# Optimization experiments

Hardware: AMD Instinct MI355X
Metric: run time of the kernel (lower is better)

The kernel has to match this reference:

```python
import jax, jax.numpy as jnp
import numpy as np

D = 512      # model_size
NH = 8       # num_heads
HD = D // NH # head_dim = 64
T = 2048     # seq len (qlen == klen == pos len)
B = 2        # batch

# flattened Bayesian parameter layout (matches flatten_list order in the module)
_SHAPES = [(3 * D, D), (D, D), (D, D), (3 * D,), (D,), (D,), (NH, HD), (NH, HD)]
_N = sum(int(np.prod(s)) for s in _SHAPES)  # 1,314,304


def _unflatten(w):
    out, i = [], 0
    for s in _SHAPES:
        n = int(np.prod(s))
        out.append(w[i:i + n].reshape(s))
        i += n
    return out


def _rel_shift(x):
    # Transformer-XL relative shift: x is [qlen, klen, B, NH]
    q, k, b, n = x.shape
    x = jnp.pad(x, ((0, 0), (1, 0), (0, 0), (0, 0)))  # zero col at front of klen axis
    x = x.reshape(k + 1, q, b, n)[1:]
    return x.reshape(q, k, b, n)


def setup_inputs() -> dict:
    key = jax.random.key(0)
    k1, k2, k3, k4, k5 = jax.random.split(key, 5)
    inp = jax.random.normal(k1, (T, B, D), dtype=jnp.float32)
    pos = jax.random.normal(k2, (T, 1, D), dtype=jnp.float32)
    std = np.sqrt(2.0 / (D + D))
    mu = jax.random.normal(k3, (_N,), dtype=jnp.float32) * std
    rho = -5.0 + 0.1 * jax.random.normal(k4, (_N,), dtype=jnp.float32)
    eps = jax.random.normal(k5, (_N,), dtype=jnp.float32)
    attn_mask = jnp.triu(jnp.ones((T, T), dtype=bool), 1)  # True = masked (future)
    return {"input": inp, "pos": pos, "attn_mask": attn_mask,
            "mu": mu, "rho": rho, "eps": eps}


def reference(input, pos, attn_mask, mu, rho, eps):
    # Gaussian reparameterized weight sample: w = mu + softplus(rho) * eps
    w = mu + jax.nn.softplus(rho) * eps
    (in_w, out_w, pos_w, in_b, out_b, pos_b, r_w_bias, r_r_bias) = _unflatten(w)

    # input projection -> q, k, v : [T, B, NH, HD]
    qkv = input @ in_w.T + in_b                      # [T, B, 3D]
    q, k, v = jnp.split(qkv, 3, axis=-1)
    q = q.reshape(T, B, NH, HD)
    k = k.reshape(T, B, NH, HD)
    v = v.reshape(T, B, NH, HD)

    # relative position projection: [R, NH, HD]
    r = (pos[:, 0, :] @ pos_w.T + pos_b).reshape(-1, NH, HD)

    # content score (AC) and position score (BD) with rel-shift
    AC = jnp.einsum('ibnd,jbnd->ijbn', q + r_w_bias, k)
    BD = _rel_shift(jnp.einsum('ibnd,jnd->ijbn', q + r_r_bias, r))

    scale = np.float32(1.0 / np.sqrt(HD))
    score = (AC + BD) * scale                        # [T, T, B, NH]
    score = jnp.where(attn_mask[:, :, None, None],
                      jnp.finfo(score.dtype).min, score)
    probs = jax.nn.softmax(score, axis=1)

    attn_vec = jnp.einsum('ijbn,jbnd->ibnd', probs, v).reshape(T, B, D)
    return attn_vec @ out_w.T + out_b                # [T, B, D]
```

## Files before the change

### kernel.cpp

```cpp
#include <hip/hip_runtime.h>


typedef float f32x4 __attribute__((ext_vector_type(4)));
typedef short bf16x8 __attribute__((ext_vector_type(8)));

#define NW 1314304
#define OFF_INB  1310720
#define OFF_INW  0
#define OFF_OUTW 786432
#define OFF_POSW 1048576
#define BB_IN  0
#define BB_OUT 1536
#define BB_POS 2048
#define BB_RW  2560
#define BB_RR  3072

#define L2E 1.44269504088896340736f

__device__ __forceinline__ unsigned short f2bf(float x) {
  unsigned u = __builtin_bit_cast(unsigned, x);
  u += 0x7fffu + ((u >> 16) & 1u);
  return (unsigned short)(u >> 16);
}
__device__ __forceinline__ float bf2f(unsigned short s) {
  return __builtin_bit_cast(float, ((unsigned)s) << 16);
}
__device__ __forceinline__ unsigned pk2(float lo, float hi) {
  return (unsigned)f2bf(lo) | ((unsigned)f2bf(hi) << 16);
}

__global__ void prep_kernel(const float* __restrict__ mu, const float* __restrict__ rho,
                            const float* __restrict__ eps,
                            const float* __restrict__ input, const float* __restrict__ pos,
                            unsigned short* __restrict__ Wh, float* __restrict__ Bf,
                            unsigned short* __restrict__ inH, unsigned short* __restrict__ posH) {
  const int bx = blockIdx.x;
  if (bx < 1284) {
    int i = (bx * 256 + threadIdx.x) * 4;
    if (i < NW) {
      float4 m = *(const float4*)&mu[i];
      float4 r = *(const float4*)&rho[i];
      float4 e = *(const float4*)&eps[i];
      float w0 = m.x + ((r.x > 20.f) ? r.x : log1pf(expf(r.x))) * e.x;
      float w1 = m.y + ((r.y > 20.f) ? r.y : log1pf(expf(r.y))) * e.y;
      float w2 = m.z + ((r.z > 20.f) ? r.z : log1pf(expf(r.z))) * e.z;
      float w3 = m.w + ((r.w > 20.f) ? r.w : log1pf(expf(r.w))) * e.w;
      union { unsigned short s[4]; uint2 u; } p;
      p.s[0] = f2bf(w0); p.s[1] = f2bf(w1); p.s[2] = f2bf(w2); p.s[3] = f2bf(w3);
      *(uint2*)&Wh[i] = p.u;
      if (i >= OFF_INB) {
        float4 b; b.x = w0; b.y = w1; b.z = w2; b.w = w3;
        *(float4*)&Bf[i - OFF_INB] = b;
      }
    }
  } else if (bx < 3332) {
    int i = ((bx - 1284) * 256 + threadIdx.x) * 4;
    float4 v = *(const float4*)&input[i];
    union { unsigned short s[4]; uint2 u; } p;
    p.s[0] = f2bf(v.x); p.s[1] = f2bf(v.y); p.s[2] = f2bf(v.z); p.s[3] = f2bf(v.w);
    *(uint2*)&inH[i] = p.u;
  } else {
    int i = ((bx - 3332) * 256 + threadIdx.x) * 4;
    float4 v = *(const float4*)&pos[i];
    union { unsigned short s[4]; uint2 u; } p;
    p.s[0] = f2bf(v.x); p.s[1] = f2bf(v.y); p.s[2] = f2bf(v.z); p.s[3] = f2bf(v.w);
    *(uint2*)&posH[i] = p.u;
  }
}

__device__ __forceinline__ void gemm_loop(const unsigned short* __restrict__ A,
                                          const unsigned short* __restrict__ B,
                                          unsigned short* As, unsigned short* Bs,
                                          f32x4 (&acc)[4]) {
  const int tid = threadIdx.x;
  const int wv = tid >> 6, lane = tid & 63, g = lane >> 4, cc = lane & 15;
  const int row = tid >> 2, q4 = tid & 3;
  const unsigned short* Ap = A + (size_t)row * 512 + 16 * q4;
  const unsigned short* Bp = B + (size_t)row * 512 + 16 * q4;

  *(uint4*)&As[row * 72 + 16 * q4]     = *(const uint4*)Ap;
  *(uint4*)&As[row * 72 + 16 * q4 + 8] = *(const uint4*)(Ap + 8);
  *(uint4*)&Bs[row * 72 + 16 * q4]     = *(const uint4*)Bp;
  *(uint4*)&Bs[row * 72 + 16 * q4 + 8] = *(const uint4*)(Bp + 8);
  __syncthreads();

  for (int it = 0; it < 8; it++) {
    uint4 a0, a1, b0, b1;
    const bool pf = (it < 7);
    if (pf) {
      const unsigned short* An = Ap + 64 * (it + 1);
      const unsigned short* Bn = Bp + 64 * (it + 1);
      a0 = *(const uint4*)An; a1 = *(const uint4*)(An + 8);
      b0 = *(const uint4*)Bn; b1 = *(const uint4*)(Bn + 8);
    }
    __builtin_amdgcn_s_setprio(1);
#pragma unroll
    for (int ks = 0; ks < 2; ks++) {
      bf16x8 af = *(const bf16x8*)&As[(16 * wv + cc) * 72 + 32 * ks + 8 * g];
#pragma unroll
      for (int fn = 0; fn < 4; fn++) {
        bf16x8 bf = *(const bf16x8*)&Bs[(16 * fn + cc) * 72 + 32 * ks + 8 * g];
        acc[fn] = __builtin_amdgcn_mfma_f32_16x16x32_bf16(af, bf, acc[fn], 0, 0, 0);
      }
    }
    __builtin_amdgcn_s_setprio(0);
    __syncthreads();
    if (pf) {
      *(uint4*)&As[row * 72 + 16 * q4]     = a0;
      *(uint4*)&As[row * 72 + 16 * q4 + 8] = a1;
      *(uint4*)&Bs[row * 72 + 16 * q4]     = b0;
      *(uint4*)&Bs[row * 72 + 16 * q4 + 8] = b1;
    }
    __syncthreads();
  }
}

__global__ __launch_bounds__(256, 2)
void gemm01_kernel(const unsigned short* __restrict__ inH, const unsigned short* __restrict__ posH,
                   const unsigned short* __restrict__ Wh, const float* __restrict__ Bf,
                   unsigned short* __restrict__ qrw, unsigned short* __restrict__ qrr,
                   unsigned short* __restrict__ kbuf, unsigned short* __restrict__ vT,
                   unsigned short* __restrict__ rbuf) {
  __shared__ __align__(16) unsigned short As[64 * 72];
  __shared__ __align__(16) unsigned short Bs[64 * 72];
  const int bx = blockIdx.x;
  const int tid = threadIdx.x;
  const int wv = tid >> 6, lane = tid & 63, g = lane >> 4, cc = lane & 15;

  const bool isR = (bx >= 1536);
  int m0, n0;
  const unsigned short *A, *W;
  if (!isR) {
    m0 = (bx & 63) << 6; n0 = (bx >> 6) << 6;
    A = inH + (size_t)m0 * 512;  W = Wh + OFF_INW + (size_t)n0 * 512;
  } else {
    const int t = bx - 1536;
    m0 = (t & 31) << 6; n0 = (t >> 5) << 6;
    A = posH + (size_t)m0 * 512; W = Wh + OFF_POSW + (size_t)n0 * 512;
  }

  f32x4 acc[4];
#pragma unroll
  for (int i = 0; i < 4; i++) { acc[i][0] = 0.f; acc[i][1] = 0.f; acc[i][2] = 0.f; acc[i][3] = 0.f; }
  gemm_loop(A, W, As, Bs, acc);

  const int sec = n0 >> 9;
  if (!isR && sec == 2) {
#pragma unroll
    for (int fn = 0; fn < 4; fn++) {
      const int col = n0 + 16 * fn + cc;
#pragma unroll
      for (int r = 0; r < 4; r++)
        As[(16 * wv + 4 * g + r) * 72 + 16 * fn + cc] = f2bf(acc[fn][r] + Bf[BB_IN + col]);
    }
    __syncthreads();
    const int nh2 = (n0 >> 6) & 7;
#pragma unroll
    for (int cpass = 0; cpass < 2; cpass++) {
      const int ch = tid + cpass * 256;
      const int ncol = ch >> 3, bb2 = (ch >> 2) & 1, jc = ch & 3;
      union { unsigned short s[8]; uint4 u; } pk;
#pragma unroll
      for (int jj = 0; jj < 8; jj++)
        pk.s[jj] = As[(2 * (8 * jc + jj) + bb2) * 72 + ncol];
      *(uint4*)&vT[((size_t)(bb2 * 8 + nh2) * 64 + ncol) * 2048 + (m0 >> 1) + 8 * jc] = pk.u;
    }
    return;
  }

#pragma unroll
  for (int fn = 0; fn < 4; fn++) {
    const int col = n0 + 16 * fn + cc;
#pragma unroll
    for (int r = 0; r < 4; r++) {
      const int mrow = m0 + 16 * wv + 4 * g + r;
      float v = acc[fn][r];
      if (!isR) {
        v += Bf[BB_IN + col];
        const int d = col & 511;
        const int nh = d >> 6, hd = d & 63;
        const int t = mrow >> 1, bb = mrow & 1;
        const size_t bi = ((size_t)(bb * 8 + nh) * 2048 + t) * 64 + hd;
        if (sec == 0) {
          qrw[bi] = f2bf(v + Bf[BB_RW + d]);
          qrr[bi] = f2bf(v + Bf[BB_RR + d]);
        } else {
          kbuf[bi] = f2bf(v);
        }
      } else {
        v += Bf[BB_POS + col];
        rbuf[((size_t)(col >> 6) * 2048 + mrow) * 64 + (col & 63)] = f2bf(v);
      }
    }
  }
}

__global__ __launch_bounds__(256, 2)
void gemmO_kernel(const unsigned short* __restrict__ av, const unsigned short* __restrict__ W,
                  const float* __restrict__ Bf, float* __restrict__ outp) {
  __shared__ __align__(16) unsigned short As[64 * 72];
  __shared__ __align__(16) unsigned short Bs[64 * 72];
  const int bx = blockIdx.x;
  const int tid = threadIdx.x;
  const int wv = tid >> 6, lane = tid & 63, g = lane >> 4, cc = lane & 15;
  const int m0 = (bx & 63) << 6, n0 = (bx >> 6) << 6;

  f32x4 acc[4];
#pragma unroll
  for (int i = 0; i < 4; i++) { acc[i][0] = 0.f; acc[i][1] = 0.f; acc[i][2] = 0.f; acc[i][3] = 0.f; }
  gemm_loop(av + (size_t)m0 * 512, W + (size_t)n0 * 512, As, Bs, acc);

#pragma unroll
  for (int fn = 0; fn < 4; fn++) {
    const int col = n0 + 16 * fn + cc;
#pragma unroll
    for (int r = 0; r < 4; r++) {
      const int mrow = m0 + 16 * wv + 4 * g + r;
      outp[(size_t)mrow * 512 + col] = acc[fn][r] + Bf[BB_OUT + col];
    }
  }
}

__global__ __launch_bounds__(256, 3)
void attn_kernel(const unsigned short* __restrict__ qrw, const unsigned short* __restrict__ qrr,
                 const unsigned short* __restrict__ kb, const unsigned short* __restrict__ vt,
                 const unsigned short* __restrict__ rb, unsigned short* __restrict__ av,
                 unsigned short* __restrict__ pO, float* __restrict__ pStats)
{
  __shared__ __align__(16) unsigned short Ks[64 * 72];
  __shared__ __align__(16) unsigned short Vs[64 * 72];
  __shared__ __align__(16) unsigned short Rs[128 * 72];
  __shared__ __align__(16) unsigned short Gs[4 * 80 * 20];

  const int tid = threadIdx.x;
  const int wv = tid >> 6, lane = tid & 63, g = lane >> 4, cc = lane & 15;
  const int bx = (int)blockIdx.x;
  const int bn = bx & 15;
  const int sid = 79 - (bx >> 4);
  int qt, s, ns;
  if (sid < 8)       { qt = sid;                s = 0;           ns = 1; }
  else if (sid < 24) { qt = 8 + ((sid - 8) >> 1); s = (sid - 8) & 1; ns = 2; }
  else if (sid < 48) { const int t = sid - 24; const int q3 = t / 3; qt = 16 + q3; s = t - 3 * q3; ns = 3; }
  else               { const int t = sid - 48; qt = 24 + (t >> 2); s = t & 3; ns = 4; }
  const int kt0 = s * 8;
  const int kt1 = (kt0 + 8 < qt + 1) ? (kt0 + 8) : (qt + 1);

  const int nh = bn & 7, bb = bn >> 3;
  const int i0 = qt * 64;
  const int i0g = i0 + wv * 16;
  const int w0base = 1984 - i0;

  const size_t qko = (size_t)bn * 2048 * 64;
  const size_t ro = (size_t)nh * 2048 * 64;

  bf16x8 qw[2], qr[2];
#pragma unroll
  for (int ks = 0; ks < 2; ks++) {
    qw[ks] = *(const bf16x8*)&qrw[qko + (size_t)(i0g + cc) * 64 + 32 * ks + 8 * g];
    qr[ks] = *(const bf16x8*)&qrr[qko + (size_t)(i0g + cc) * 64 + 32 * ks + 8 * g];
  }

  float m_run = -3.0e38f, l_run = 0.f;
  f32x4 o[4];
#pragma unroll
  for (int i = 0; i < 4; i++) { o[i][0] = 0.f; o[i][1] = 0.f; o[i][2] = 0.f; o[i][3] = 0.f; }

  const int srow = tid >> 2, sq = tid & 3;
  const int rrow = tid >> 1, rhalf = tid & 1;
  unsigned short* Gw = &Gs[wv * 1600];
  const int rbase = 48 - 16 * wv;

  {
    const unsigned short* kp = &kb[qko + (size_t)(kt0 * 64 + srow) * 64 + 16 * sq];
    *(uint4*)&Ks[srow * 72 + 16 * sq]     = *(const uint4*)kp;
    *(uint4*)&Ks[srow * 72 + 16 * sq + 8] = *(const uint4*)(kp + 8);
    const unsigned short* vp = &vt[qko + (size_t)srow * 2048 + kt0 * 64 + 16 * sq];
    *(uint4*)&Vs[srow * 72 + 16 * sq]     = *(const uint4*)vp;
    *(uint4*)&Vs[srow * 72 + 16 * sq + 8] = *(const uint4*)(vp + 8);
    const int u0 = w0base + kt0 * 64 + rrow;
    const int uc0 = u0 > 2047 ? 2047 : u0;
    const unsigned short* rp = &rb[ro + (size_t)uc0 * 64 + 32 * rhalf];
    unsigned short* rd = &Rs[(u0 & 127) * 72 + 32 * rhalf];
    *(uint4*)rd        = *(const uint4*)rp;
    *(uint4*)(rd + 8)  = *(const uint4*)(rp + 8);
    *(uint4*)(rd + 16) = *(const uint4*)(rp + 16);
    *(uint4*)(rd + 24) = *(const uint4*)(rp + 24);
  }
  __syncthreads();

  for (int kt = kt0; kt < kt1; kt++) {
    const int j0 = kt * 64;
    const int w0k = w0base + j0;
    const bool pf = (kt + 1 < kt1);

    uint4 ka0, ka1, va0, va1, ra0, ra1;
    int rslot = 0;
    if (pf) {
      const unsigned short* kp = &kb[qko + (size_t)(j0 + 64 + srow) * 64 + 16 * sq];
      ka0 = *(const uint4*)kp; ka1 = *(const uint4*)(kp + 8);
      const unsigned short* vp = &vt[qko + (size_t)srow * 2048 + j0 + 64 + 16 * sq];
      va0 = *(const uint4*)vp; va1 = *(const uint4*)(vp + 8);
      const int unew = w0k + 128 + (tid >> 2);
      rslot = unew & 127;
      const int uc = unew > 2047 ? 2047 : unew;
      const unsigned short* rp = &rb[ro + (size_t)uc * 64 + 16 * sq];
      ra0 = *(const uint4*)rp; ra1 = *(const uint4*)(rp + 8);
    }

    f32x4 st[4];
#pragma unroll
    for (int i = 0; i < 4; i++) { st[i][0] = 0.f; st[i][1] = 0.f; st[i][2] = 0.f; st[i][3] = 0.f; }
    __builtin_amdgcn_s_setprio(1);
#pragma unroll
    for (int ks = 0; ks < 2; ks++) {
#pragma unroll
      for (int fm = 0; fm < 4; fm++) {
        bf16x8 ka = *(const bf16x8*)&Ks[(16 * fm + cc) * 72 + 32 * ks + 8 * g];
        st[fm] = __builtin_amdgcn_mfma_f32_16x16x32_bf16(ka, qw[ks], st[fm], 0, 0, 0);
      }
    }
    f32x4 gt[5];
#pragma unroll
    for (int i = 0; i < 5; i++) { gt[i][0] = 0.f; gt[i][1] = 0.f; gt[i][2] = 0.f; gt[i][3] = 0.f; }
    const int rr0 = w0k + rbase + cc;
#pragma unroll
    for (int ks = 0; ks < 2; ks++) {
#pragma unroll
      for (int fm = 0; fm < 5; fm++) {
        const int rrw = (rr0 + 16 * fm) & 127;
        bf16x8 ra = *(const bf16x8*)&Rs[rrw * 72 + 32 * ks + 8 * g];
        gt[fm] = __builtin_amdgcn_mfma_f32_16x16x32_bf16(ra, qr[ks], gt[fm], 0, 0, 0);
      }
    }
    __builtin_amdgcn_s_setprio(0);
#pragma unroll
    for (int fm = 0; fm < 5; fm++)
#pragma unroll
      for (int r = 0; r < 4; r++)
        Gw[(16 * fm + 4 * g + r) * 20 + cc] = f2bf(gt[fm][r]);

    float p[4][4];
    float tm = -3.0e38f;
    const bool diag = (kt == qt);
#pragma unroll
    for (int fm = 0; fm < 4; fm++) {
#pragma unroll
      for (int r = 0; r < 4; r++) {
        const int jj = 16 * fm + 4 * g + r;
        float bd = bf2f(Gw[(jj - cc + 15) * 20 + cc]);
        float sv = (st[fm][r] + bd) * 0.125f;
        if (diag && (jj > cc + 16 * wv)) sv = -3.0e38f;
        p[fm][r] = sv;
        tm = fmaxf(tm, sv);
      }
    }
    tm = fmaxf(tm, __shfl_xor(tm, 16));
    tm = fmaxf(tm, __shfl_xor(tm, 32));
    const float m_new = fmaxf(m_run, tm);
    const float sc = exp2f((m_run - m_new) * L2E);
    float ps = 0.f;
#pragma unroll
    for (int fm = 0; fm < 4; fm++)
#pragma unroll
      for (int r = 0; r < 4; r++) {
        float pv = exp2f((p[fm][r] - m_new) * L2E);
        p[fm][r] = pv;
        ps += pv;
      }
    ps += __shfl_xor(ps, 16);
    ps += __shfl_xor(ps, 32);
    l_run = l_run * sc + ps;
    m_run = m_new;

    float scr[4];
#pragma unroll
    for (int r = 0; r < 4; r++) scr[r] = __shfl(sc, 4 * g + r);
#pragma unroll
    for (int fn = 0; fn < 4; fn++)
#pragma unroll
      for (int r = 0; r < 4; r++) o[fn][r] *= scr[r];

    unsigned u01[4], u23[4];
#pragma unroll
    for (int fm = 0; fm < 4; fm++) {
      u01[fm] = pk2(p[fm][0], p[fm][1]);
      u23[fm] = pk2(p[fm][2], p[fm][3]);
    }
    bf16x8 pa[2];
#pragma unroll
    for (int ks = 0; ks < 2; ks++) {
      union { unsigned u[4]; bf16x8 v; } pw;
#pragma unroll
      for (int j = 0; j < 4; j++) {
        const int srcl = (2 * (g & 1) + (j >> 1)) * 16 + cc;
        unsigned v0 = __shfl((j & 1) ? u23[2 * ks] : u01[2 * ks], srcl);
        unsigned v1 = __shfl((j & 1) ? u23[2 * ks + 1] : u01[2 * ks + 1], srcl);
        pw.u[j] = (g >> 1) ? v1 : v0;
      }
      pa[ks] = pw.v;
    }
    __builtin_amdgcn_s_setprio(1);
#pragma unroll
    for (int ks = 0; ks < 2; ks++) {
#pragma unroll
      for (int fn = 0; fn < 4; fn++) {
        bf16x8 vb = *(const bf16x8*)&Vs[(16 * fn + cc) * 72 + 32 * ks + 8 * g];
        o[fn] = __builtin_amdgcn_mfma_f32_16x16x32_bf16(pa[ks], vb, o[fn], 0, 0, 0);
      }
    }
    __builtin_amdgcn_s_setprio(0);

    __syncthreads();
    if (pf) {
      *(uint4*)&Ks[srow * 72 + 16 * sq]     = ka0;
      *(uint4*)&Ks[srow * 72 + 16 * sq + 8] = ka1;
      *(uint4*)&Vs[srow * 72 + 16 * sq]     = va0;
      *(uint4*)&Vs[srow * 72 + 16 * sq + 8] = va1;
      unsigned short* rd = &Rs[rslot * 72 + 16 * sq];
      *(uint4*)rd       = ra0;
      *(uint4*)(rd + 8) = ra1;
    }
    __syncthreads();
  }

  if (ns == 1) {
    const float inv = 1.0f / l_run;
    float invr[4];
#pragma unroll
    for (int r = 0; r < 4; r++) invr[r] = __shfl(inv, 4 * g + r);
#pragma unroll
    for (int fn = 0; fn < 4; fn++) {
      const int hd = 16 * fn + cc;
#pragma unroll
      for (int r = 0; r < 4; r++) {
        const int irow = i0g + 4 * g + r;
        av[((size_t)(irow * 2 + bb) * 8 + nh) * 64 + hd] = f2bf(o[fn][r] * invr[r]);
      }
    }
  } else {
    const size_t slot = (size_t)(bn * 80 + sid);
#pragma unroll
    for (int fn = 0; fn < 4; fn++) {
      const int hd = 16 * fn + cc;
#pragma unroll
      for (int r = 0; r < 4; r++)
        pO[slot * 4096 + (16 * wv + 4 * g + r) * 64 + hd] = f2bf(o[fn][r]);
    }
    if (g == 0) {
      pStats[slot * 128 + (16 * wv + cc) * 2]     = m_run;
      pStats[slot * 128 + (16 * wv + cc) * 2 + 1] = l_run;
    }
  }
}

__global__ __launch_bounds__(256)
void combine_kernel(const unsigned short* __restrict__ pO, const float* __restrict__ pStats,
                    unsigned short* __restrict__ av) {
  const int bxx = (int)blockIdx.x;
  const int bn = bxx & 15, qt = 8 + (bxx >> 4);
  const int nh = bn & 7, bb = bn >> 3;
  const int ns = (qt >> 3) + 1;
  const int sid0 = (qt < 16) ? (8 + (qt - 8) * 2)
                 : (qt < 24) ? (24 + (qt - 16) * 3)
                             : (48 + (qt - 24) * 4);
  const int tid = threadIdx.x;
  const int ql = tid >> 2, hq = tid & 3;
  const size_t sb = (size_t)(bn * 80 + sid0);

  float M = -3.0e38f;
  for (int i = 0; i < ns; i++)
    M = fmaxf(M, pStats[(sb + i) * 128 + ql * 2]);

  float L = 0.f;
  float accv[16];
#pragma unroll
  for (int j = 0; j < 16; j++) accv[j] = 0.f;
  for (int i = 0; i < ns; i++) {
    const float mi = pStats[(sb + i) * 128 + ql * 2];
    const float li = pStats[(sb + i) * 128 + ql * 2 + 1];
    const float w = exp2f((mi - M) * L2E);
    L += w * li;
    union { uint4 u; unsigned short s[8]; } c0, c1;
    const unsigned short* src = &pO[(sb + i) * 4096 + ql * 64 + 16 * hq];
    c0.u = *(const uint4*)src;
    c1.u = *(const uint4*)(src + 8);
#pragma unroll
    for (int j = 0; j < 8; j++) accv[j]     += w * bf2f(c0.s[j]);
#pragma unroll
    for (int j = 0; j < 8; j++) accv[8 + j] += w * bf2f(c1.s[j]);
  }
  const float inv = 1.0f / L;
  union { uint4 u; unsigned short s[8]; } o0, o1;
#pragma unroll
  for (int j = 0; j < 8; j++) o0.s[j] = f2bf(accv[j] * inv);
#pragma unroll
  for (int j = 0; j < 8; j++) o1.s[j] = f2bf(accv[8 + j] * inv);
  const int q = qt * 64 + ql;
  unsigned short* dst = &av[((size_t)(q * 2 + bb) * 8 + nh) * 64 + 16 * hq];
  *(uint4*)dst       = o0.u;
  *(uint4*)(dst + 8) = o1.u;
}

extern "C" void kernel_launch(void* const* d_in, const int* in_sizes, int n_in,
                              void* d_out, int out_size, void* d_ws, size_t ws_size,
                              hipStream_t stream) {
  const float* input = (const float*)d_in[0];
  const float* pos   = (const float*)d_in[1];
  const float* mu  = (const float*)d_in[3];
  const float* rho = (const float*)d_in[4];
  const float* eps = (const float*)d_in[5];
  float* out = (float*)d_out;

  char* ws = (char*)d_ws;
  unsigned short* Wh   = (unsigned short*)ws;
  float*          Bf   = (float*)(ws + 2628608);
  unsigned short* inH  = (unsigned short*)(ws + 2642944);
  unsigned short* posH = (unsigned short*)(ws + 6837248);
  unsigned short* qrw  = (unsigned short*)(ws + 8934400);
  unsigned short* qrr  = (unsigned short*)(ws + 13128704);
  unsigned short* kbuf = (unsigned short*)(ws + 17323008);
  unsigned short* vT   = (unsigned short*)(ws + 21517312);
  unsigned short* rbuf = (unsigned short*)(ws + 25711616);
  unsigned short* pO   = (unsigned short*)(ws + 27808768);
  float*          pSt  = (float*)(ws + 38294528);
  unsigned short* av   = inH;

  prep_kernel<<<dim3(4356), dim3(256), 0, stream>>>(mu, rho, eps, input, pos, Wh, Bf, inH, posH);
  gemm01_kernel<<<dim3(1792), dim3(256), 0, stream>>>(inH, posH, Wh, Bf, qrw, qrr, kbuf, vT, rbuf);
  attn_kernel<<<dim3(1280), dim3(256), 0, stream>>>(qrw, qrr, kbuf, vT, rbuf, av, pO, pSt);
  combine_kernel<<<dim3(384), dim3(256), 0, stream>>>(pO, pSt, av);
  gemmO_kernel<<<dim3(512), dim3(256), 0, stream>>>(av, Wh + OFF_OUTW, Bf, out);
}
```

Measured before the change: 174.6 us.

## Stage QKV/R epilogue through LDS and swap shuffles for LDS relayout in attention

The projection GEMM epilogue now writes q (with both position biases), k and r tiles into shared memory first and then stores them with coalesced 16-byte writes, in place of scattered 2-byte stores. The 1/sqrt(d) scale is folded into the q tensors there, so the attention inner loop no longer multiplies scores. In the attention kernel the BD tile is stored transposed with packed 8-byte writes and read back with 32-bit loads plus a shift for the relative offset. The P-matrix relayout for the PV MFMA now goes through per-wave LDS instead of many cross-lane shuffles. The cost is extra LDS traffic, a barrier in the epilogue, and a slightly different rounding point because the scale is applied before the bf16 conversion.

```diff
diff --git a/kernel.cpp b/kernel.cpp
--- a/kernel.cpp
+++ b/kernel.cpp
@@ -144,17 +144,63 @@
   for (int i = 0; i < 4; i++) { acc[i][0] = 0.f; acc[i][1] = 0.f; acc[i][2] = 0.f; acc[i][3] = 0.f; }
   gemm_loop(A, W, As, Bs, acc);
 
-  const int sec = n0 >> 9;
-  if (!isR && sec == 2) {
+  const int nh2 = (n0 >> 6) & 7;
+  const int sec = isR ? 3 : (n0 >> 9);
+
+  if (sec == 0) {
 #pragma unroll
     for (int fn = 0; fn < 4; fn++) {
       const int col = n0 + 16 * fn + cc;
+      const float b0 = Bf[BB_IN + col];
+      const float brw = Bf[BB_RW + col], brr = Bf[BB_RR + col];
+#pragma unroll
+      for (int r = 0; r < 4; r++) {
+        const int ml = 16 * wv + 4 * g + r;
+        As[ml * 72 + 16 * fn + cc] = f2bf((acc[fn][r] + b0 + brw) * 0.125f);
+        Bs[ml * 72 + 16 * fn + cc] = f2bf((acc[fn][r] + b0 + brr) * 0.125f);
+      }
+    }
+    __syncthreads();
+    const int t0 = m0 >> 1;
+#pragma unroll
+    for (int pass = 0; pass < 2; pass++) {
+      const int ch = tid + pass * 256;
+      const int bb2 = ch >> 8, tl = (ch >> 3) & 31, hc = ch & 7;
+      const int ml = 2 * tl + bb2;
+      uint4 v1 = *(const uint4*)&As[ml * 72 + 8 * hc];
+      uint4 v2 = *(const uint4*)&Bs[ml * 72 + 8 * hc];
+      const size_t dst = ((size_t)(bb2 * 8 + nh2) * 2048 + t0 + tl) * 64 + 8 * hc;
+      *(uint4*)&qrw[dst] = v1;
+      *(uint4*)&qrr[dst] = v2;
+    }
+  } else if (sec == 1) {
+#pragma unroll
+    for (int fn = 0; fn < 4; fn++) {
+      const int col = n0 + 16 * fn + cc;
+      const float b0 = Bf[BB_IN + col];
+#pragma unroll
+      for (int r = 0; r < 4; r++)
+        As[(16 * wv + 4 * g + r) * 72 + 16 * fn + cc] = f2bf(acc[fn][r] + b0);
+    }
+    __syncthreads();
+    const int t0 = m0 >> 1;
+#pragma unroll
+    for (int pass = 0; pass < 2; pass++) {
+      const int ch = tid + pass * 256;
+      const int bb2 = ch >> 8, tl = (ch >> 3) & 31, hc = ch & 7;
+      const int ml = 2 * tl + bb2;
+      uint4 v1 = *(const uint4*)&As[ml * 72 + 8 * hc];
+      *(uint4*)&kbuf[((size_t)(bb2 * 8 + nh2) * 2048 + t0 + tl) * 64 + 8 * hc] = v1;
+    }
+  } else if (sec == 2) {
+#pragma unroll
+    for (int fn = 0; fn < 4; fn++) {
+      const int col = n0 + 16 * fn + cc;
 #pragma unroll
       for (int r = 0; r < 4; r++)
         As[(16 * wv + 4 * g + r) * 72 + 16 * fn + cc] = f2bf(acc[fn][r] + Bf[BB_IN + col]);
     }
     __syncthreads();
-    const int nh2 = (n0 >> 6) & 7;
 #pragma unroll
     for (int cpass = 0; cpass < 2; cpass++) {
       const int ch = tid + cpass * 256;
@@ -165,32 +211,22 @@
         pk.s[jj] = As[(2 * (8 * jc + jj) + bb2) * 72 + ncol];
       *(uint4*)&vT[((size_t)(bb2 * 8 + nh2) * 64 + ncol) * 2048 + (m0 >> 1) + 8 * jc] = pk.u;
     }
-    return;
-  }
-
-#pragma unroll
-  for (int fn = 0; fn < 4; fn++) {
-    const int col = n0 + 16 * fn + cc;
-#pragma unroll
-    for (int r = 0; r < 4; r++) {
-      const int mrow = m0 + 16 * wv + 4 * g + r;
-      float v = acc[fn][r];
-      if (!isR) {
-        v += Bf[BB_IN + col];
-        const int d = col & 511;
-        const int nh = d >> 6, hd = d & 63;
-        const int t = mrow >> 1, bb = mrow & 1;
-        const size_t bi = ((size_t)(bb * 8 + nh) * 2048 + t) * 64 + hd;
-        if (sec == 0) {
-          qrw[bi] = f2bf(v + Bf[BB_RW + d]);
-          qrr[bi] = f2bf(v + Bf[BB_RR + d]);
-        } else {
-          kbuf[bi] = f2bf(v);
-        }
-      } else {
-        v += Bf[BB_POS + col];
-        rbuf[((size_t)(col >> 6) * 2048 + mrow) * 64 + (col & 63)] = f2bf(v);
-      }
+  } else {
+#pragma unroll
+    for (int fn = 0; fn < 4; fn++) {
+      const int col = n0 + 16 * fn + cc;
+      const float b0 = Bf[BB_POS + col];
+#pragma unroll
+      for (int r = 0; r < 4; r++)
+        As[(16 * wv + 4 * g + r) * 72 + 16 * fn + cc] = f2bf(acc[fn][r] + b0);
+    }
+    __syncthreads();
+#pragma unroll
+    for (int pass = 0; pass < 2; pass++) {
+      const int ch = tid + pass * 256;
+      const int ml = ch >> 3, hc = ch & 7;
+      uint4 v1 = *(const uint4*)&As[ml * 72 + 8 * hc];
+      *(uint4*)&rbuf[((size_t)nh2 * 2048 + m0 + ml) * 64 + 8 * hc] = v1;
     }
   }
 }
@@ -230,7 +266,7 @@
   __shared__ __align__(16) unsigned short Ks[64 * 72];
   __shared__ __align__(16) unsigned short Vs[64 * 72];
   __shared__ __align__(16) unsigned short Rs[128 * 72];
-  __shared__ __align__(16) unsigned short Gs[4 * 80 * 20];
+  __shared__ __align__(16) unsigned short GPs[4 * 16 * 84];
 
   const int tid = threadIdx.x;
   const int wv = tid >> 6, lane = tid & 63, g = lane >> 4, cc = lane & 15;
@@ -267,7 +303,7 @@
 
   const int srow = tid >> 2, sq = tid & 3;
   const int rrow = tid >> 1, rhalf = tid & 1;
-  unsigned short* Gw = &Gs[wv * 1600];
+  unsigned short* Gw = &GPs[wv * 1344];
   const int rbase = 48 - 16 * wv;
 
   {
@@ -333,26 +369,48 @@
       }
     }
     __builtin_amdgcn_s_setprio(0);
-#pragma unroll
-    for (int fm = 0; fm < 5; fm++)
-#pragma unroll
-      for (int r = 0; r < 4; r++)
-        Gw[(16 * fm + 4 * g + r) * 20 + cc] = f2bf(gt[fm][r]);
+
+#pragma unroll
+    for (int fm = 0; fm < 5; fm++) {
+      uint2 w;
+      w.x = pk2(gt[fm][0], gt[fm][1]);
+      w.y = pk2(gt[fm][2], gt[fm][3]);
+      *(uint2*)&Gw[cc * 84 + 16 * fm + 4 * g] = w;
+    }
 
     float p[4][4];
     float tm = -3.0e38f;
     const bool diag = (kt == qt);
+    const int c00 = 15 - cc + 4 * g;
 #pragma unroll
     for (int fm = 0; fm < 4; fm++) {
-#pragma unroll
-      for (int r = 0; r < 4; r++) {
-        const int jj = 16 * fm + 4 * g + r;
-        float bd = bf2f(Gw[(jj - cc + 15) * 20 + cc]);
-        float sv = (st[fm][r] + bd) * 0.125f;
-        if (diag && (jj > cc + 16 * wv)) sv = -3.0e38f;
-        p[fm][r] = sv;
-        tm = fmaxf(tm, sv);
-      }
+      const int c0 = c00 + 16 * fm;
+      const int e0 = c0 & ~1;
+      const unsigned short* gp = &Gw[cc * 84 + e0];
+      unsigned d0 = *(const unsigned*)gp;
+      unsigned d1 = *(const unsigned*)(gp + 2);
+      unsigned d2 = *(const unsigned*)(gp + 4);
+      unsigned lo01, lo23;
+      if (c0 & 1) { lo01 = (d0 >> 16) | (d1 << 16); lo23 = (d1 >> 16) | (d2 << 16); }
+      else        { lo01 = d0; lo23 = d1; }
+      float bd0 = bf2f((unsigned short)(lo01 & 0xffffu));
+      float bd1 = bf2f((unsigned short)(lo01 >> 16));
+      float bd2 = bf2f((unsigned short)(lo23 & 0xffffu));
+      float bd3 = bf2f((unsigned short)(lo23 >> 16));
+      float sv0 = st[fm][0] + bd0;
+      float sv1 = st[fm][1] + bd1;
+      float sv2 = st[fm][2] + bd2;
+      float sv3 = st[fm][3] + bd3;
+      if (diag) {
+        const int jj = 16 * fm + 4 * g;
+        const int lim = cc + 16 * wv;
+        if (jj + 0 > lim) sv0 = -3.0e38f;
+        if (jj + 1 > lim) sv1 = -3.0e38f;
+        if (jj + 2 > lim) sv2 = -3.0e38f;
+        if (jj + 3 > lim) sv3 = -3.0e38f;
+      }
+      p[fm][0] = sv0; p[fm][1] = sv1; p[fm][2] = sv2; p[fm][3] = sv3;
+      tm = fmaxf(tm, fmaxf(fmaxf(sv0, sv1), fmaxf(sv2, sv3)));
     }
     tm = fmaxf(tm, __shfl_xor(tm, 16));
     tm = fmaxf(tm, __shfl_xor(tm, 32));
@@ -380,25 +438,18 @@
 #pragma unroll
       for (int r = 0; r < 4; r++) o[fn][r] *= scr[r];
 
-    unsigned u01[4], u23[4];
 #pragma unroll
     for (int fm = 0; fm < 4; fm++) {
-      u01[fm] = pk2(p[fm][0], p[fm][1]);
-      u23[fm] = pk2(p[fm][2], p[fm][3]);
+      uint2 w;
+      w.x = pk2(p[fm][0], p[fm][1]);
+      w.y = pk2(p[fm][2], p[fm][3]);
+      *(uint2*)&Gw[cc * 72 + 16 * fm + 4 * g] = w;
     }
     bf16x8 pa[2];
 #pragma unroll
-    for (int ks = 0; ks < 2; ks++) {
-      union { unsigned u[4]; bf16x8 v; } pw;
-#pragma unroll
-      for (int j = 0; j < 4; j++) {
-        const int srcl = (2 * (g & 1) + (j >> 1)) * 16 + cc;
-        unsigned v0 = __shfl((j & 1) ? u23[2 * ks] : u01[2 * ks], srcl);
-        unsigned v1 = __shfl((j & 1) ? u23[2 * ks + 1] : u01[2 * ks + 1], srcl);
-        pw.u[j] = (g >> 1) ? v1 : v0;
-      }
-      pa[ks] = pw.v;
-    }
+    for (int ks = 0; ks < 2; ks++)
+      pa[ks] = *(const bf16x8*)&Gw[cc * 72 + 32 * ks + 8 * g];
+
     __builtin_amdgcn_s_setprio(1);
 #pragma unroll
     for (int ks = 0; ks < 2; ks++) {
```

Result: no change. 171.5 us (-1.8%).
